# Optimization experiments

Hardware: AMD Instinct MI355X
Metric: run time of the kernel (lower is better)

Reference implementation:

```python
import jax, jax.numpy as jnp
import numpy as np

# Straight-through-estimator sign: forward sign(x), backward identity.
@jax.custom_vjp
def ste_sign(x):
    return jnp.sign(x)

def _ste_fwd(x):
    return jnp.sign(x), None

def _ste_bwd(_, g):
    return (g,)

ste_sign.defvjp(_ste_fwd, _ste_bwd)

D_MODEL = 2048
D_HIDDEN = 8192

def setup_inputs() -> dict:
    key = jax.random.key(0)
    k_x, k_up, k_dn = jax.random.split(key, 3)
    x = jax.random.normal(k_x, (2, 2048, D_MODEL), dtype=jnp.float32)
    up_weight = jax.random.normal(k_up, (D_HIDDEN, D_MODEL), dtype=jnp.float32) * 0.02
    down_weight = jax.random.normal(k_dn, (D_MODEL, D_HIDDEN), dtype=jnp.float32) * 0.02
    up_scale = jnp.ones((D_HIDDEN,), dtype=jnp.float32)
    down_scale = jnp.ones((D_MODEL,), dtype=jnp.float32)
    output_scale = jnp.ones((1,), dtype=jnp.float32)
    return {"x": x, "up_weight": up_weight, "down_weight": down_weight,
            "up_scale": up_scale, "down_scale": down_scale, "output_scale": output_scale}

def reference(x, up_weight, down_weight, up_scale, down_scale, output_scale):
    up_w = ste_sign(up_weight)      # [d_hidden, d_model], ternary {-1,0,1}
    down_w = ste_sign(down_weight)  # [d_model, d_hidden]
    # F.linear(x, W) == x @ W.T
    hidden = jnp.einsum('bsd,hd->bsh', x, up_w) * up_scale
    hidden = jax.nn.relu(hidden)
    out = jnp.einsum('bsh,dh->bsd', hidden, down_w) * down_scale
    return out * output_scale
```

## Files before the change

### kernel.cpp

```cpp
#include <hip/hip_runtime.h>
#include <stdint.h>


#define M_TOK 4096
#define DM 2048
#define DH 8192

typedef __attribute__((ext_vector_type(4))) int i32x4;
typedef __attribute__((ext_vector_type(4))) float f32x4;
typedef __attribute__((ext_vector_type(8))) unsigned short u16x8;

__device__ __forceinline__ ushort f2bf_rne(float f) {
  union { float f; uint32_t u; } c; c.f = f;
  uint32_t u = c.u;
  uint32_t r = (u + 0x7FFFu + ((u >> 16) & 1u)) >> 16;
  return (ushort)r;
}

__device__ __forceinline__ float bf2f(ushort u) {
  union { uint32_t u; float f; } c; c.u = (uint32_t)u << 16;
  return c.f;
}

#define GLD16(g, l)                                                     \
  __builtin_amdgcn_global_load_lds(                                     \
      (const __attribute__((address_space(1))) void*)(g),               \
      (__attribute__((address_space(3))) void*)(l), 16, 0, 0)

#define FENCE() asm volatile("" ::: "memory")

__global__ __launch_bounds__(256) void quantx_kernel(
    const float* __restrict__ x, int8_t* __restrict__ xq,
    float* __restrict__ sx) {
  const int row = blockIdx.x, tid = threadIdx.x;
  const float4* xr = (const float4*)(x + (size_t)row * 2048);
  float4 a = xr[tid * 2], b = xr[tid * 2 + 1];
  float m = fmaxf(fmaxf(fmaxf(fabsf(a.x), fabsf(a.y)), fmaxf(fabsf(a.z), fabsf(a.w))),
                  fmaxf(fmaxf(fabsf(b.x), fabsf(b.y)), fmaxf(fabsf(b.z), fabsf(b.w))));
#pragma unroll
  for (int off = 32; off >= 1; off >>= 1) m = fmaxf(m, __shfl_xor(m, off));
  __shared__ float red[4];
  if ((tid & 63) == 0) red[tid >> 6] = m;
  __syncthreads();
  m = fmaxf(fmaxf(red[0], red[1]), fmaxf(red[2], red[3]));
  const float inv = m > 0.f ? 127.f / m : 0.f;
  if (tid == 0) sx[row] = m > 0.f ? m / 127.f : 0.f;
  auto q8 = [&](float v) -> uint32_t {
    float q = rintf(v * inv);
    q = fminf(fmaxf(q, -127.f), 127.f);
    return (uint32_t)(uint8_t)(int8_t)(int)q;
  };
  uint32_t w0 = q8(a.x) | (q8(a.y) << 8) | (q8(a.z) << 16) | (q8(a.w) << 24);
  uint32_t w1 = q8(b.x) | (q8(b.y) << 8) | (q8(b.z) << 16) | (q8(b.w) << 24);
  uint32_t* o = (uint32_t*)(xq + (size_t)row * 2048);
  o[tid * 2] = w0;
  o[tid * 2 + 1] = w1;
}

__global__ void signq_kernel(const float* __restrict__ in,
                             int8_t* __restrict__ out, int n4) {
  int stride = gridDim.x * blockDim.x;
  auto s8 = [](float v) -> uint32_t {
    int s = (v > 0.f) - (v < 0.f);
    return (uint32_t)(uint8_t)(int8_t)s;
  };
  for (int i = blockIdx.x * blockDim.x + threadIdx.x; i < n4; i += stride) {
    float4 v = ((const float4*)in)[i];
    ((uint32_t*)out)[i] = s8(v.x) | (s8(v.y) << 8) | (s8(v.z) << 16) | (s8(v.w) << 24);
  }
}

__global__ __launch_bounds__(256) void quanth_kernel(
    const ushort* __restrict__ hid, int8_t* __restrict__ hq,
    float* __restrict__ sh) {
  const int row = blockIdx.x, tid = threadIdx.x;
  const u16x8* hr = (const u16x8*)(hid + (size_t)row * 8192);
  u16x8 h[4];
  float m = 0.f;
#pragma unroll
  for (int s = 0; s < 4; ++s) {
    h[s] = hr[tid * 4 + s];
#pragma unroll
    for (int j = 0; j < 8; ++j) m = fmaxf(m, fabsf(bf2f(h[s][j])));
  }
#pragma unroll
  for (int off = 32; off >= 1; off >>= 1) m = fmaxf(m, __shfl_xor(m, off));
  __shared__ float red[4];
  if ((tid & 63) == 0) red[tid >> 6] = m;
  __syncthreads();
  m = fmaxf(fmaxf(red[0], red[1]), fmaxf(red[2], red[3]));
  const float inv = m > 0.f ? 127.f / m : 0.f;
  if (tid == 0) sh[row] = m > 0.f ? m / 127.f : 0.f;
  auto q8 = [&](float v) -> uint32_t {
    float q = rintf(v * inv);
    q = fminf(fmaxf(q, -127.f), 127.f);
    return (uint32_t)(uint8_t)(int8_t)(int)q;
  };
  uint32_t* o = (uint32_t*)(hq + (size_t)row * 8192);
#pragma unroll
  for (int s = 0; s < 4; ++s) {
    uint32_t w0 = q8(bf2f(h[s][0])) | (q8(bf2f(h[s][1])) << 8) |
                  (q8(bf2f(h[s][2])) << 16) | (q8(bf2f(h[s][3])) << 24);
    uint32_t w1 = q8(bf2f(h[s][4])) | (q8(bf2f(h[s][5])) << 8) |
                  (q8(bf2f(h[s][6])) << 16) | (q8(bf2f(h[s][7])) << 24);
    o[tid * 8 + s * 2] = w0;
    o[tid * 8 + s * 2 + 1] = w1;
  }
}

__global__ __launch_bounds__(512, 2) void gemm1_i8_kernel(
    const int8_t* __restrict__ A, const int8_t* __restrict__ B,
    ushort* __restrict__ C, const float* __restrict__ sx,
    const float* __restrict__ ups, int M, int N, int K) {
  constexpr int TILEB = 256 * 128;
  constexpr int BUFB = 2 * TILEB;
  extern __shared__ char smem[];

  const int nbn = N >> 8;
  const int bid = blockIdx.x;
  const int cpx = gridDim.x >> 3;
  const int swz = (bid & 7) * cpx + (bid >> 3);
  const int bm = swz / nbn, bn = swz % nbn;

  const int tid = threadIdx.x;
  const int lane = tid & 63;
  const int wv = tid >> 6;
  const int wm = wv >> 2, wn = wv & 3;
  const int lr = lane & 15, lg = lane >> 4;

  const int srow = tid >> 3;
  const int scolB = ((tid & 7) ^ (srow & 7)) << 4;
  const int8_t* aS = A + (size_t)(bm * 256 + srow) * K + scolB;
  const int8_t* bS = B + (size_t)(bn * 256 + srow) * K + scolB;
  const int ldsl = wv * 1024;

  auto STAGE = [&](int t, int u) {
    char* dst = smem + (t & 1) * BUFB + u * 8192 + ldsl;
    const int8_t* src = (u < 4) ? aS + (size_t)(u * 64) * K + (size_t)t * 128
                                : bS + (size_t)((u - 4) * 64) * K + (size_t)t * 128;
    GLD16(src, dst);
  };

  const int nt = K >> 7;
  i32x4 acc[8][4] = {};

#pragma unroll
  for (int u = 0; u < 8; ++u) STAGE(0, u);
  if (nt > 1) {
    STAGE(1, 0); STAGE(1, 2); STAGE(1, 4); STAGE(1, 5);
    asm volatile("s_waitcnt vmcnt(4)" ::: "memory");
  } else {
    asm volatile("s_waitcnt vmcnt(0)" ::: "memory");
  }
  __builtin_amdgcn_s_barrier();

  const int xorv = (lr & 7) << 4;
  const int k0 = (lg << 4) ^ xorv;
  const int k1 = (64 + (lg << 4)) ^ xorv;
  const int abase = (wm * 128 + lr) * 128;
  const int bbase = TILEB + (wn * 64 + lr) * 128;

#define MFMA_G(Q, p, q, r, s)                                                \
  __builtin_amdgcn_s_setprio(1);                                             \
  _Pragma("unroll") for (int fc = 0; fc < 4; ++fc)                           \
      acc[2*(Q)][fc] = __builtin_amdgcn_mfma_i32_16x16x64_i8(                \
          p, b0[fc], acc[2*(Q)][fc], 0, 0, 0);                               \
  _Pragma("unroll") for (int fc = 0; fc < 4; ++fc)                           \
      acc[2*(Q)+1][fc] = __builtin_amdgcn_mfma_i32_16x16x64_i8(              \
          r, b0[fc], acc[2*(Q)+1][fc], 0, 0, 0);                             \
  _Pragma("unroll") for (int fc = 0; fc < 4; ++fc)                           \
      acc[2*(Q)][fc] = __builtin_amdgcn_mfma_i32_16x16x64_i8(                \
          q, b1[fc], acc[2*(Q)][fc], 0, 0, 0);                               \
  _Pragma("unroll") for (int fc = 0; fc < 4; ++fc)                           \
      acc[2*(Q)+1][fc] = __builtin_amdgcn_mfma_i32_16x16x64_i8(              \
          s, b1[fc], acc[2*(Q)+1][fc], 0, 0, 0);                             \
  __builtin_amdgcn_s_setprio(0);

#define WAITL(n)                                               \
  asm volatile("s_waitcnt lgkmcnt(" #n ")" ::: "memory");      \
  __builtin_amdgcn_sched_barrier(0);

  for (int t = 0; t < nt; ++t) {
    const char* bufc = smem + (t & 1) * BUFB;
    const char* bA = bufc + abase;
    const char* bB = bufc + bbase;
    i32x4 b0[4], b1[4];
    i32x4 p0, p1, p2, p3, q0, q1, q2, q3;

    p0 = *(const i32x4*)(bA + 0 * 2048 + k0);
    p1 = *(const i32x4*)(bA + 0 * 2048 + k1);
    p2 = *(const i32x4*)(bA + 1 * 2048 + k0);
    p3 = *(const i32x4*)(bA + 1 * 2048 + k1);
#pragma unroll
    for (int fc = 0; fc < 4; ++fc) {
      b0[fc] = *(const i32x4*)(bB + fc * 2048 + k0);
      b1[fc] = *(const i32x4*)(bB + fc * 2048 + k1);
    }
    FENCE();
    q0 = *(const i32x4*)(bA + 2 * 2048 + k0);
    q1 = *(const i32x4*)(bA + 2 * 2048 + k1);
    q2 = *(const i32x4*)(bA + 3 * 2048 + k0);
    q3 = *(const i32x4*)(bA + 3 * 2048 + k1);
    FENCE();
    if (t + 1 < nt) { STAGE(t + 1, 6); STAGE(t + 1, 7);
                      STAGE(t + 1, 1); STAGE(t + 1, 3); }
    WAITL(4);
    MFMA_G(0, p0, p1, p2, p3);
    p0 = *(const i32x4*)(bA + 4 * 2048 + k0);
    p1 = *(const i32x4*)(bA + 4 * 2048 + k1);
    p2 = *(const i32x4*)(bA + 5 * 2048 + k0);
    p3 = *(const i32x4*)(bA + 5 * 2048 + k1);
    FENCE();
    WAITL(4);
    MFMA_G(1, q0, q1, q2, q3);
    q0 = *(const i32x4*)(bA + 6 * 2048 + k0);
    q1 = *(const i32x4*)(bA + 6 * 2048 + k1);
    q2 = *(const i32x4*)(bA + 7 * 2048 + k0);
    q3 = *(const i32x4*)(bA + 7 * 2048 + k1);
    FENCE();
    WAITL(4);
    MFMA_G(2, p0, p1, p2, p3);
    WAITL(0);
    MFMA_G(3, q0, q1, q2, q3);

    __builtin_amdgcn_s_barrier();
    if (t + 2 < nt) { STAGE(t + 2, 0); STAGE(t + 2, 2);
                      STAGE(t + 2, 4); STAGE(t + 2, 5); }
    if (t + 2 < nt) {
      asm volatile("s_waitcnt vmcnt(4)" ::: "memory");
    } else {
      asm volatile("s_waitcnt vmcnt(0)" ::: "memory");
    }
    __builtin_amdgcn_s_barrier();
  }
#undef MFMA_G
#undef WAITL

  float uc[4];
#pragma unroll
  for (int fc = 0; fc < 4; ++fc) uc[fc] = ups[bn * 256 + wn * 64 + fc * 16 + lr];
#pragma unroll
  for (int fr = 0; fr < 8; ++fr) {
    int gr = bm * 256 + wm * 128 + fr * 16 + lg * 4;
    float4 sxv = *(const float4*)(sx + gr);
#pragma unroll
    for (int fc = 0; fc < 4; ++fc) {
      int gcol = bn * 256 + wn * 64 + fc * 16 + lr;
      float s0 = sxv.x, s1 = sxv.y, s2 = sxv.z, s3 = sxv.w;
      float v0 = (float)acc[fr][fc][0] * s0 * uc[fc];
      float v1 = (float)acc[fr][fc][1] * s1 * uc[fc];
      float v2 = (float)acc[fr][fc][2] * s2 * uc[fc];
      float v3 = (float)acc[fr][fc][3] * s3 * uc[fc];
      C[(size_t)(gr + 0) * N + gcol] = f2bf_rne(v0 > 0.f ? v0 : 0.f);
      C[(size_t)(gr + 1) * N + gcol] = f2bf_rne(v1 > 0.f ? v1 : 0.f);
      C[(size_t)(gr + 2) * N + gcol] = f2bf_rne(v2 > 0.f ? v2 : 0.f);
      C[(size_t)(gr + 3) * N + gcol] = f2bf_rne(v3 > 0.f ? v3 : 0.f);
    }
  }
}

__global__ __launch_bounds__(512, 2) void gemm2_i8_kernel(
    const int8_t* __restrict__ A, const int8_t* __restrict__ B,
    float* __restrict__ C, const float* __restrict__ sh,
    const float* __restrict__ dns, const float* __restrict__ oscale,
    int M, int N, int K) {
  constexpr int ABYTES = 256 * 128;
  constexpr int BBYTES = 128 * 128;
  constexpr int BUFB = ABYTES + BBYTES;
  extern __shared__ char smem[];

  const int nbn = N >> 7;
  const int bid = blockIdx.x;
  const int cpx = gridDim.x >> 3;
  const int swz = (bid & 7) * cpx + (bid >> 3);
  const int bm = swz / nbn, bn = swz % nbn;

  const int tid = threadIdx.x;
  const int lane = tid & 63;
  const int wv = tid >> 6;
  const int wm = wv >> 1, wn = wv & 1;
  const int lr = lane & 15, lg = lane >> 4;

  const int srow = tid >> 3;
  const int scolB = ((tid & 7) ^ (srow & 7)) << 4;
  const int8_t* aS = A + (size_t)(bm * 256 + srow) * K + scolB;
  const int8_t* bS = B + (size_t)(bn * 128 + srow) * K + scolB;
  const int ldsl = wv * 1024;

  i32x4 acc[4][4] = {};
  const int nt = K >> 7;

  auto STAGE = [&](int t, int q) {
    char* dA = smem + q * BUFB;
    char* dB = dA + ABYTES;
    const int8_t* a0 = aS + (size_t)t * 128;
    const int8_t* b0 = bS + (size_t)t * 128;
#pragma unroll
    for (int a = 0; a < 4; ++a)
      GLD16(a0 + (size_t)(a * 64) * K, dA + a * 8192 + ldsl);
#pragma unroll
    for (int b = 0; b < 2; ++b)
      GLD16(b0 + (size_t)(b * 64) * K, dB + b * 8192 + ldsl);
  };

  STAGE(0, 0);
  STAGE(1, 1);
  asm volatile("s_waitcnt vmcnt(6)" ::: "memory");
  __builtin_amdgcn_s_barrier();

  const int xorv = (lr & 7) << 4;
  int cur = 0;
  for (int t = 0; t < nt; ++t) {
    int nx = cur + 2; nx = (nx >= 3) ? nx - 3 : nx;
    if (t + 2 < nt) STAGE(t + 2, nx);

    const char* cA = smem + cur * BUFB;
    const char* cB = cA + ABYTES;
    i32x4 af[2][4], bfr[2][4];
#pragma unroll
    for (int ks = 0; ks < 2; ++ks) {
      int ko = ((ks << 6) + (lg << 4)) ^ xorv;
#pragma unroll
      for (int i = 0; i < 4; ++i)
        af[ks][i] = *(const i32x4*)(cA + ((wm * 64 + i * 16 + lr) << 7) + ko);
#pragma unroll
      for (int j = 0; j < 4; ++j)
        bfr[ks][j] = *(const i32x4*)(cB + ((wn * 64 + j * 16 + lr) << 7) + ko);
    }

    __builtin_amdgcn_s_setprio(1);
#pragma unroll
    for (int ks = 0; ks < 2; ++ks)
#pragma unroll
      for (int i = 0; i < 4; ++i)
#pragma unroll
        for (int j = 0; j < 4; ++j)
          acc[i][j] = __builtin_amdgcn_mfma_i32_16x16x64_i8(
              af[ks][i], bfr[ks][j], acc[i][j], 0, 0, 0);
    __builtin_amdgcn_s_setprio(0);

    if (t + 2 < nt) {
      asm volatile("s_waitcnt vmcnt(6)" ::: "memory");
    } else if (t + 1 < nt) {
      asm volatile("s_waitcnt vmcnt(0)" ::: "memory");
    }
    __builtin_amdgcn_s_barrier();
    cur = cur + 1; if (cur == 3) cur = 0;
  }

  float osc_v = oscale[0];
  float dc[4];
#pragma unroll
  for (int j = 0; j < 4; ++j)
    dc[j] = dns[bn * 128 + wn * 64 + j * 16 + lr] * osc_v;
#pragma unroll
  for (int i = 0; i < 4; ++i) {
    int gr = bm * 256 + wm * 64 + i * 16 + lg * 4;
    float4 shv = *(const float4*)(sh + gr);
#pragma unroll
    for (int j = 0; j < 4; ++j) {
      int gcol = bn * 128 + wn * 64 + j * 16 + lr;
      C[(size_t)(gr + 0) * N + gcol] = (float)acc[i][j][0] * shv.x * dc[j];
      C[(size_t)(gr + 1) * N + gcol] = (float)acc[i][j][1] * shv.y * dc[j];
      C[(size_t)(gr + 2) * N + gcol] = (float)acc[i][j][2] * shv.z * dc[j];
      C[(size_t)(gr + 3) * N + gcol] = (float)acc[i][j][3] * shv.w * dc[j];
    }
  }
}

extern "C" void kernel_launch(void* const* d_in, const int* in_sizes, int n_in,
                              void* d_out, int out_size, void* d_ws,
                              size_t ws_size, hipStream_t stream) {
  const float* x   = (const float*)d_in[0];
  const float* upw = (const float*)d_in[1];
  const float* dnw = (const float*)d_in[2];
  const float* ups = (const float*)d_in[3];
  const float* dns = (const float*)d_in[4];
  const float* osc = (const float*)d_in[5];
  float* out = (float*)d_out;

  char* ws = (char*)d_ws;
  int8_t* xq  = (int8_t*)(ws);
  int8_t* upq = (int8_t*)(ws + 8388608);
  int8_t* dnq = (int8_t*)(ws + 25165824);
  ushort* hid = (ushort*)(ws + 41943040);
  int8_t* hq  = (int8_t*)(ws + 109051904);
  float*  sx  = (float*)(ws + 142606336);
  float*  sh  = (float*)(ws + 142622720);

  quantx_kernel<<<M_TOK, 256, 0, stream>>>(x, xq, sx);
  signq_kernel<<<2048, 256, 0, stream>>>(upw, upq, (DH * DM) / 4);
  signq_kernel<<<2048, 256, 0, stream>>>(dnw, dnq, (DM * DH) / 4);

  const int smem1 = 131072;
  const int smem2 = 147456;
  (void)hipFuncSetAttribute(reinterpret_cast<const void*>(gemm1_i8_kernel),
                            hipFuncAttributeMaxDynamicSharedMemorySize, smem1);
  (void)hipFuncSetAttribute(reinterpret_cast<const void*>(gemm2_i8_kernel),
                            hipFuncAttributeMaxDynamicSharedMemorySize, smem2);

  gemm1_i8_kernel<<<(M_TOK / 256) * (DH / 256), 512, smem1, stream>>>(
      xq, upq, hid, sx, ups, M_TOK, DH, DM);
  quanth_kernel<<<M_TOK, 256, 0, stream>>>(hid, hq, sh);
  gemm2_i8_kernel<<<(M_TOK / 256) * (DM / 128), 512, smem2, stream>>>(
      hq, dnq, out, sh, dns, osc, M_TOK, DM, DH);
}
```

Before: 203.8 us.

## Pre-pack sign weights into MFMA fragment layout and load B directly from global

The sign-quantization kernel now writes weights in a per-tile, per-lane MFMA fragment order, so the GEMMs can load B operands straight from global memory into registers without LDS staging. Both GEMMs are unified into one templated 128x128-tile kernel with 256 threads and only A double-buffered in static LDS, targeting higher occupancy (3 blocks per CU) and lower LDS traffic. The trade-off is smaller tiles with less reuse, global-latency-exposed B loads without prefetch, and the loss of the hand-tuned 256x256 gemm1 pipeline.

After: 229.0 us. 1.12x slower.

```diff
diff --git a/kernel.cpp b/kernel.cpp
--- a/kernel.cpp
+++ b/kernel.cpp
@@ -7,7 +7,6 @@
 #define DH 8192
 
 typedef __attribute__((ext_vector_type(4))) int i32x4;
-typedef __attribute__((ext_vector_type(4))) float f32x4;
 typedef __attribute__((ext_vector_type(8))) unsigned short u16x8;
 
 __device__ __forceinline__ ushort f2bf_rne(float f) {
@@ -57,16 +56,30 @@
   o[tid * 2 + 1] = w1;
 }
 
-__global__ void signq_kernel(const float* __restrict__ in,
-                             int8_t* __restrict__ out, int n4) {
-  int stride = gridDim.x * blockDim.x;
+__global__ __launch_bounds__(256) void signfrag_kernel(
+    const float* __restrict__ W, int8_t* __restrict__ Bp, int Kd, int nt) {
+  const int bid = blockIdx.x;
+  const int cb = bid / nt, t = bid % nt;
+  const int tid = threadIdx.x;
+  int8_t* dst0 = Bp + ((size_t)bid << 14);
   auto s8 = [](float v) -> uint32_t {
     int s = (v > 0.f) - (v < 0.f);
     return (uint32_t)(uint8_t)(int8_t)s;
   };
-  for (int i = blockIdx.x * blockDim.x + threadIdx.x; i < n4; i += stride) {
-    float4 v = ((const float4*)in)[i];
-    ((uint32_t*)out)[i] = s8(v.x) | (s8(v.y) << 8) | (s8(v.z) << 16) | (s8(v.w) << 24);
+#pragma unroll
+  for (int i = 0; i < 4; ++i) {
+    int c = tid + 256 * i;
+    int l = c & 63, fc = (c >> 6) & 3, ks = (c >> 8) & 1, wn = c >> 9;
+    int row = cb * 128 + wn * 64 + fc * 16 + (l & 15);
+    int kb = t * 128 + ks * 64 + ((l >> 4) << 4);
+    const float4* src = (const float4*)(W + (size_t)row * Kd + kb);
+    uint32_t w[4];
+#pragma unroll
+    for (int j = 0; j < 4; ++j) {
+      float4 v = src[j];
+      w[j] = s8(v.x) | (s8(v.y) << 8) | (s8(v.z) << 16) | (s8(v.w) << 24);
+    }
+    *(uint4*)(dst0 + (size_t)c * 16) = make_uint4(w[0], w[1], w[2], w[3]);
   }
 }
 
@@ -108,166 +121,14 @@
   }
 }
 
-__global__ __launch_bounds__(512, 2) void gemm1_i8_kernel(
-    const int8_t* __restrict__ A, const int8_t* __restrict__ B,
-    ushort* __restrict__ C, const float* __restrict__ sx,
-    const float* __restrict__ ups, int M, int N, int K) {
-  constexpr int TILEB = 256 * 128;
-  constexpr int BUFB = 2 * TILEB;
-  extern __shared__ char smem[];
-
-  const int nbn = N >> 8;
-  const int bid = blockIdx.x;
-  const int cpx = gridDim.x >> 3;
-  const int swz = (bid & 7) * cpx + (bid >> 3);
-  const int bm = swz / nbn, bn = swz % nbn;
-
-  const int tid = threadIdx.x;
-  const int lane = tid & 63;
-  const int wv = tid >> 6;
-  const int wm = wv >> 2, wn = wv & 3;
-  const int lr = lane & 15, lg = lane >> 4;
-
-  const int srow = tid >> 3;
-  const int scolB = ((tid & 7) ^ (srow & 7)) << 4;
-  const int8_t* aS = A + (size_t)(bm * 256 + srow) * K + scolB;
-  const int8_t* bS = B + (size_t)(bn * 256 + srow) * K + scolB;
-  const int ldsl = wv * 1024;
-
-  auto STAGE = [&](int t, int u) {
-    char* dst = smem + (t & 1) * BUFB + u * 8192 + ldsl;
-    const int8_t* src = (u < 4) ? aS + (size_t)(u * 64) * K + (size_t)t * 128
-                                : bS + (size_t)((u - 4) * 64) * K + (size_t)t * 128;
-    GLD16(src, dst);
-  };
-
-  const int nt = K >> 7;
-  i32x4 acc[8][4] = {};
-
-#pragma unroll
-  for (int u = 0; u < 8; ++u) STAGE(0, u);
-  if (nt > 1) {
-    STAGE(1, 0); STAGE(1, 2); STAGE(1, 4); STAGE(1, 5);
-    asm volatile("s_waitcnt vmcnt(4)" ::: "memory");
-  } else {
-    asm volatile("s_waitcnt vmcnt(0)" ::: "memory");
-  }
-  __builtin_amdgcn_s_barrier();
-
-  const int xorv = (lr & 7) << 4;
-  const int k0 = (lg << 4) ^ xorv;
-  const int k1 = (64 + (lg << 4)) ^ xorv;
-  const int abase = (wm * 128 + lr) * 128;
-  const int bbase = TILEB + (wn * 64 + lr) * 128;
-
-#define MFMA_G(Q, p, q, r, s)                                                \
-  __builtin_amdgcn_s_setprio(1);                                             \
-  _Pragma("unroll") for (int fc = 0; fc < 4; ++fc)                           \
-      acc[2*(Q)][fc] = __builtin_amdgcn_mfma_i32_16x16x64_i8(                \
-          p, b0[fc], acc[2*(Q)][fc], 0, 0, 0);                               \
-  _Pragma("unroll") for (int fc = 0; fc < 4; ++fc)                           \
-      acc[2*(Q)+1][fc] = __builtin_amdgcn_mfma_i32_16x16x64_i8(              \
-          r, b0[fc], acc[2*(Q)+1][fc], 0, 0, 0);                             \
-  _Pragma("unroll") for (int fc = 0; fc < 4; ++fc)                           \
-      acc[2*(Q)][fc] = __builtin_amdgcn_mfma_i32_16x16x64_i8(                \
-          q, b1[fc], acc[2*(Q)][fc], 0, 0, 0);                               \
-  _Pragma("unroll") for (int fc = 0; fc < 4; ++fc)                           \
-      acc[2*(Q)+1][fc] = __builtin_amdgcn_mfma_i32_16x16x64_i8(              \
-          s, b1[fc], acc[2*(Q)+1][fc], 0, 0, 0);                             \
-  __builtin_amdgcn_s_setprio(0);
-
-#define WAITL(n)                                               \
-  asm volatile("s_waitcnt lgkmcnt(" #n ")" ::: "memory");      \
-  __builtin_amdgcn_sched_barrier(0);
-
-  for (int t = 0; t < nt; ++t) {
-    const char* bufc = smem + (t & 1) * BUFB;
-    const char* bA = bufc + abase;
-    const char* bB = bufc + bbase;
-    i32x4 b0[4], b1[4];
-    i32x4 p0, p1, p2, p3, q0, q1, q2, q3;
-
-    p0 = *(const i32x4*)(bA + 0 * 2048 + k0);
-    p1 = *(const i32x4*)(bA + 0 * 2048 + k1);
-    p2 = *(const i32x4*)(bA + 1 * 2048 + k0);
-    p3 = *(const i32x4*)(bA + 1 * 2048 + k1);
-#pragma unroll
-    for (int fc = 0; fc < 4; ++fc) {
-      b0[fc] = *(const i32x4*)(bB + fc * 2048 + k0);
-      b1[fc] = *(const i32x4*)(bB + fc * 2048 + k1);
-    }
-    FENCE();
-    q0 = *(const i32x4*)(bA + 2 * 2048 + k0);
-    q1 = *(const i32x4*)(bA + 2 * 2048 + k1);
-    q2 = *(const i32x4*)(bA + 3 * 2048 + k0);
-    q3 = *(const i32x4*)(bA + 3 * 2048 + k1);
-    FENCE();
-    if (t + 1 < nt) { STAGE(t + 1, 6); STAGE(t + 1, 7);
-                      STAGE(t + 1, 1); STAGE(t + 1, 3); }
-    WAITL(4);
-    MFMA_G(0, p0, p1, p2, p3);
-    p0 = *(const i32x4*)(bA + 4 * 2048 + k0);
-    p1 = *(const i32x4*)(bA + 4 * 2048 + k1);
-    p2 = *(const i32x4*)(bA + 5 * 2048 + k0);
-    p3 = *(const i32x4*)(bA + 5 * 2048 + k1);
-    FENCE();
-    WAITL(4);
-    MFMA_G(1, q0, q1, q2, q3);
-    q0 = *(const i32x4*)(bA + 6 * 2048 + k0);
-    q1 = *(const i32x4*)(bA + 6 * 2048 + k1);
-    q2 = *(const i32x4*)(bA + 7 * 2048 + k0);
-    q3 = *(const i32x4*)(bA + 7 * 2048 + k1);
-    FENCE();
-    WAITL(4);
-    MFMA_G(2, p0, p1, p2, p3);
-    WAITL(0);
-    MFMA_G(3, q0, q1, q2, q3);
-
-    __builtin_amdgcn_s_barrier();
-    if (t + 2 < nt) { STAGE(t + 2, 0); STAGE(t + 2, 2);
-                      STAGE(t + 2, 4); STAGE(t + 2, 5); }
-    if (t + 2 < nt) {
-      asm volatile("s_waitcnt vmcnt(4)" ::: "memory");
-    } else {
-      asm volatile("s_waitcnt vmcnt(0)" ::: "memory");
-    }
-    __builtin_amdgcn_s_barrier();
-  }
-#undef MFMA_G
-#undef WAITL
-
-  float uc[4];
-#pragma unroll
-  for (int fc = 0; fc < 4; ++fc) uc[fc] = ups[bn * 256 + wn * 64 + fc * 16 + lr];
-#pragma unroll
-  for (int fr = 0; fr < 8; ++fr) {
-    int gr = bm * 256 + wm * 128 + fr * 16 + lg * 4;
-    float4 sxv = *(const float4*)(sx + gr);
-#pragma unroll
-    for (int fc = 0; fc < 4; ++fc) {
-      int gcol = bn * 256 + wn * 64 + fc * 16 + lr;
-      float s0 = sxv.x, s1 = sxv.y, s2 = sxv.z, s3 = sxv.w;
-      float v0 = (float)acc[fr][fc][0] * s0 * uc[fc];
-      float v1 = (float)acc[fr][fc][1] * s1 * uc[fc];
-      float v2 = (float)acc[fr][fc][2] * s2 * uc[fc];
-      float v3 = (float)acc[fr][fc][3] * s3 * uc[fc];
-      C[(size_t)(gr + 0) * N + gcol] = f2bf_rne(v0 > 0.f ? v0 : 0.f);
-      C[(size_t)(gr + 1) * N + gcol] = f2bf_rne(v1 > 0.f ? v1 : 0.f);
-      C[(size_t)(gr + 2) * N + gcol] = f2bf_rne(v2 > 0.f ? v2 : 0.f);
-      C[(size_t)(gr + 3) * N + gcol] = f2bf_rne(v3 > 0.f ? v3 : 0.f);
-    }
-  }
-}
-
-__global__ __launch_bounds__(512, 2) void gemm2_i8_kernel(
-    const int8_t* __restrict__ A, const int8_t* __restrict__ B,
-    float* __restrict__ C, const float* __restrict__ sh,
-    const float* __restrict__ dns, const float* __restrict__ oscale,
+template <int EPI>
+__global__ __launch_bounds__(256, 3) void gemm_bd_kernel(
+    const int8_t* __restrict__ A, const int8_t* __restrict__ Bp,
+    void* __restrict__ Cv, const float* __restrict__ rs,
+    const float* __restrict__ cs, const float* __restrict__ os,
     int M, int N, int K) {
-  constexpr int ABYTES = 256 * 128;
-  constexpr int BBYTES = 128 * 128;
-  constexpr int BUFB = ABYTES + BBYTES;
-  extern __shared__ char smem[];
+  constexpr int TILEA = 128 * 128;
+  __shared__ __align__(16) char smem[2 * TILEA];
 
   const int nbn = N >> 7;
   const int bid = blockIdx.x;
@@ -283,87 +144,127 @@
 
   const int srow = tid >> 3;
   const int scolB = ((tid & 7) ^ (srow & 7)) << 4;
-  const int8_t* aS = A + (size_t)(bm * 256 + srow) * K + scolB;
-  const int8_t* bS = B + (size_t)(bn * 128 + srow) * K + scolB;
+  const int8_t* aS = A + (size_t)(bm * 128 + srow) * K + scolB;
   const int ldsl = wv * 1024;
+  const int nt = K >> 7;
+
+  auto ASTAGE = [&](int t) {
+    char* dst = smem + ((t & 1) ? TILEA : 0) + ldsl;
+    const int8_t* src = aS + (size_t)t * 128;
+#pragma unroll
+    for (int u = 0; u < 4; ++u)
+      GLD16(src + (size_t)(u * 32) * K, dst + u * 4096);
+  };
 
   i32x4 acc[4][4] = {};
-  const int nt = K >> 7;
-
-  auto STAGE = [&](int t, int q) {
-    char* dA = smem + q * BUFB;
-    char* dB = dA + ABYTES;
-    const int8_t* a0 = aS + (size_t)t * 128;
-    const int8_t* b0 = bS + (size_t)t * 128;
-#pragma unroll
-    for (int a = 0; a < 4; ++a)
-      GLD16(a0 + (size_t)(a * 64) * K, dA + a * 8192 + ldsl);
-#pragma unroll
-    for (int b = 0; b < 2; ++b)
-      GLD16(b0 + (size_t)(b * 64) * K, dB + b * 8192 + ldsl);
-  };
-
-  STAGE(0, 0);
-  STAGE(1, 1);
-  asm volatile("s_waitcnt vmcnt(6)" ::: "memory");
+
+  ASTAGE(0);
+  asm volatile("s_waitcnt vmcnt(0)" ::: "memory");
   __builtin_amdgcn_s_barrier();
 
   const int xorv = (lr & 7) << 4;
-  int cur = 0;
+  const int k0 = (lg << 4) ^ xorv;
+  const int k1 = (64 + (lg << 4)) ^ xorv;
+  const int abase = (wm * 64 + lr) * 128;
+  const size_t bwave = (size_t)((wn * 2) * 4) * 1024 + (size_t)lane * 16;
+
   for (int t = 0; t < nt; ++t) {
-    int nx = cur + 2; nx = (nx >= 3) ? nx - 3 : nx;
-    if (t + 2 < nt) STAGE(t + 2, nx);
-
-    const char* cA = smem + cur * BUFB;
-    const char* cB = cA + ABYTES;
-    i32x4 af[2][4], bfr[2][4];
-#pragma unroll
-    for (int ks = 0; ks < 2; ++ks) {
-      int ko = ((ks << 6) + (lg << 4)) ^ xorv;
-#pragma unroll
-      for (int i = 0; i < 4; ++i)
-        af[ks][i] = *(const i32x4*)(cA + ((wm * 64 + i * 16 + lr) << 7) + ko);
-#pragma unroll
-      for (int j = 0; j < 4; ++j)
-        bfr[ks][j] = *(const i32x4*)(cB + ((wn * 64 + j * 16 + lr) << 7) + ko);
-    }
-
+    const int8_t* bTile = Bp + (((size_t)bn * nt + t) << 14);
+    i32x4 b0[4], b1[4];
+#pragma unroll
+    for (int fc = 0; fc < 4; ++fc) {
+      b0[fc] = *(const i32x4*)(bTile + bwave + (size_t)fc * 1024);
+      b1[fc] = *(const i32x4*)(bTile + bwave + 4096 + (size_t)fc * 1024);
+    }
+    FENCE();
+
+    const char* bA = smem + ((t & 1) ? TILEA : 0) + abase;
+    i32x4 a0[4], a1[4];
+#pragma unroll
+    for (int fr = 0; fr < 4; ++fr) a0[fr] = *(const i32x4*)(bA + fr * 2048 + k0);
+    FENCE();
+#pragma unroll
+    for (int fr = 0; fr < 4; ++fr) a1[fr] = *(const i32x4*)(bA + fr * 2048 + k1);
+    FENCE();
+
+    if (t + 1 < nt) ASTAGE(t + 1);
+
+    if (t + 1 < nt) {
+      asm volatile("s_waitcnt vmcnt(4)" ::: "memory");
+    } else {
+      asm volatile("s_waitcnt vmcnt(0)" ::: "memory");
+    }
+    __builtin_amdgcn_sched_barrier(0);
+
+    asm volatile("s_waitcnt lgkmcnt(4)" ::: "memory");
+    __builtin_amdgcn_sched_barrier(0);
     __builtin_amdgcn_s_setprio(1);
 #pragma unroll
-    for (int ks = 0; ks < 2; ++ks)
-#pragma unroll
-      for (int i = 0; i < 4; ++i)
-#pragma unroll
-        for (int j = 0; j < 4; ++j)
-          acc[i][j] = __builtin_amdgcn_mfma_i32_16x16x64_i8(
-              af[ks][i], bfr[ks][j], acc[i][j], 0, 0, 0);
+    for (int fr = 0; fr < 4; ++fr)
+#pragma unroll
+      for (int fc = 0; fc < 4; ++fc)
+        acc[fr][fc] = __builtin_amdgcn_mfma_i32_16x16x64_i8(
+            a0[fr], b0[fc], acc[fr][fc], 0, 0, 0);
     __builtin_amdgcn_s_setprio(0);
 
-    if (t + 2 < nt) {
-      asm volatile("s_waitcnt vmcnt(6)" ::: "memory");
-    } else if (t + 1 < nt) {
+    asm volatile("s_waitcnt lgkmcnt(0)" ::: "memory");
+    __builtin_amdgcn_sched_barrier(0);
+    __builtin_amdgcn_s_setprio(1);
+#pragma unroll
+    for (int fr = 0; fr < 4; ++fr)
+#pragma unroll
+      for (int fc = 0; fc < 4; ++fc)
+        acc[fr][fc] = __builtin_amdgcn_mfma_i32_16x16x64_i8(
+            a1[fr], b1[fc], acc[fr][fc], 0, 0, 0);
+    __builtin_amdgcn_s_setprio(0);
+
+    if (t + 1 < nt) {
       asm volatile("s_waitcnt vmcnt(0)" ::: "memory");
-    }
-    __builtin_amdgcn_s_barrier();
-    cur = cur + 1; if (cur == 3) cur = 0;
-  }
-
-  float osc_v = oscale[0];
-  float dc[4];
-#pragma unroll
-  for (int j = 0; j < 4; ++j)
-    dc[j] = dns[bn * 128 + wn * 64 + j * 16 + lr] * osc_v;
-#pragma unroll
-  for (int i = 0; i < 4; ++i) {
-    int gr = bm * 256 + wm * 64 + i * 16 + lg * 4;
-    float4 shv = *(const float4*)(sh + gr);
-#pragma unroll
-    for (int j = 0; j < 4; ++j) {
-      int gcol = bn * 128 + wn * 64 + j * 16 + lr;
-      C[(size_t)(gr + 0) * N + gcol] = (float)acc[i][j][0] * shv.x * dc[j];
-      C[(size_t)(gr + 1) * N + gcol] = (float)acc[i][j][1] * shv.y * dc[j];
-      C[(size_t)(gr + 2) * N + gcol] = (float)acc[i][j][2] * shv.z * dc[j];
-      C[(size_t)(gr + 3) * N + gcol] = (float)acc[i][j][3] * shv.w * dc[j];
+      __builtin_amdgcn_s_barrier();
+    }
+  }
+
+  if (EPI == 0) {
+    ushort* C = (ushort*)Cv;
+    float cc[4];
+#pragma unroll
+    for (int fc = 0; fc < 4; ++fc) cc[fc] = cs[bn * 128 + wn * 64 + fc * 16 + lr];
+#pragma unroll
+    for (int fr = 0; fr < 4; ++fr) {
+      int gr = bm * 128 + wm * 64 + fr * 16 + lg * 4;
+      float4 rv = *(const float4*)(rs + gr);
+#pragma unroll
+      for (int fc = 0; fc < 4; ++fc) {
+        int gcol = bn * 128 + wn * 64 + fc * 16 + lr;
+        float v0 = (float)acc[fr][fc][0] * rv.x * cc[fc];
+        float v1 = (float)acc[fr][fc][1] * rv.y * cc[fc];
+        float v2 = (float)acc[fr][fc][2] * rv.z * cc[fc];
+        float v3 = (float)acc[fr][fc][3] * rv.w * cc[fc];
+        C[(size_t)(gr + 0) * N + gcol] = f2bf_rne(v0 > 0.f ? v0 : 0.f);
+        C[(size_t)(gr + 1) * N + gcol] = f2bf_rne(v1 > 0.f ? v1 : 0.f);
+        C[(size_t)(gr + 2) * N + gcol] = f2bf_rne(v2 > 0.f ? v2 : 0.f);
+        C[(size_t)(gr + 3) * N + gcol] = f2bf_rne(v3 > 0.f ? v3 : 0.f);
+      }
+    }
+  } else {
+    float* C = (float*)Cv;
+    float osv = os[0];
+    float cc[4];
+#pragma unroll
+    for (int fc = 0; fc < 4; ++fc)
+      cc[fc] = cs[bn * 128 + wn * 64 + fc * 16 + lr] * osv;
+#pragma unroll
+    for (int fr = 0; fr < 4; ++fr) {
+      int gr = bm * 128 + wm * 64 + fr * 16 + lg * 4;
+      float4 rv = *(const float4*)(rs + gr);
+#pragma unroll
+      for (int fc = 0; fc < 4; ++fc) {
+        int gcol = bn * 128 + wn * 64 + fc * 16 + lr;
+        C[(size_t)(gr + 0) * N + gcol] = (float)acc[fr][fc][0] * rv.x * cc[fc];
+        C[(size_t)(gr + 1) * N + gcol] = (float)acc[fr][fc][1] * rv.y * cc[fc];
+        C[(size_t)(gr + 2) * N + gcol] = (float)acc[fr][fc][2] * rv.z * cc[fc];
+        C[(size_t)(gr + 3) * N + gcol] = (float)acc[fr][fc][3] * rv.w * cc[fc];
+      }
     }
   }
 }
@@ -381,27 +282,20 @@
 
   char* ws = (char*)d_ws;
   int8_t* xq  = (int8_t*)(ws);
-  int8_t* upq = (int8_t*)(ws + 8388608);
-  int8_t* dnq = (int8_t*)(ws + 25165824);
+  int8_t* upb = (int8_t*)(ws + 8388608);
+  int8_t* dnb = (int8_t*)(ws + 25165824);
   ushort* hid = (ushort*)(ws + 41943040);
   int8_t* hq  = (int8_t*)(ws + 109051904);
   float*  sx  = (float*)(ws + 142606336);
   float*  sh  = (float*)(ws + 142622720);
 
   quantx_kernel<<<M_TOK, 256, 0, stream>>>(x, xq, sx);
-  signq_kernel<<<2048, 256, 0, stream>>>(upw, upq, (DH * DM) / 4);
-  signq_kernel<<<2048, 256, 0, stream>>>(dnw, dnq, (DM * DH) / 4);
-
-  const int smem1 = 131072;
-  const int smem2 = 147456;
-  (void)hipFuncSetAttribute(reinterpret_cast<const void*>(gemm1_i8_kernel),
-                            hipFuncAttributeMaxDynamicSharedMemorySize, smem1);
-  (void)hipFuncSetAttribute(reinterpret_cast<const void*>(gemm2_i8_kernel),
-                            hipFuncAttributeMaxDynamicSharedMemorySize, smem2);
-
-  gemm1_i8_kernel<<<(M_TOK / 256) * (DH / 256), 512, smem1, stream>>>(
-      xq, upq, hid, sx, ups, M_TOK, DH, DM);
+  signfrag_kernel<<<(DH / 128) * (DM / 128), 256, 0, stream>>>(upw, upb, DM, DM / 128);
+  signfrag_kernel<<<(DM / 128) * (DH / 128), 256, 0, stream>>>(dnw, dnb, DH, DH / 128);
+
+  gemm_bd_kernel<0><<<(M_TOK / 128) * (DH / 128), 256, 0, stream>>>(
+      xq, upb, (void*)hid, sx, ups, nullptr, M_TOK, DH, DM);
   quanth_kernel<<<M_TOK, 256, 0, stream>>>(hid, hq, sh);
-  gemm2_i8_kernel<<<(M_TOK / 256) * (DM / 128), 512, smem2, stream>>>(
-      hq, dnq, out, sh, dns, osc, M_TOK, DM, DH);
-}
+  gemm_bd_kernel<1><<<(M_TOK / 128) * (DM / 128), 256, 0, stream>>>(
+      hq, dnb, out, sh, dns, osc, M_TOK, DM, DH);
+}
```
